# Kernel optimization log

Hardware: AMD Instinct MI355X
Metric: run time of the kernel (lower is better)

The kernel has to match this reference:

```python
import jax, jax.numpy as jnp
import numpy as np
from jax import lax

B, N, IN_DIM = 8, 196, 2048
C = 256          # conv_channels / subspace dim
G = 1            # relation_glimpse


def _dilated_conv(x, w, b, dil):
    # x: [B,N,N,Cin], w: [3,3,Cin,Cout], SAME padding, rhs dilation per source
    y = lax.conv_general_dilated(x, w, window_strides=(1, 1), padding='SAME',
                                 rhs_dilation=dil,
                                 dimension_numbers=('NHWC', 'HWIO', 'NHWC'))
    return y + b


def _rel_map(X):
    # X: [B,N,N,G] -> symmetric add, move glimpse to axis 1, softmax over N*N
    Xs = X + jnp.transpose(X, (0, 2, 1, 3))          # [B,N,N,G]
    m = jnp.transpose(Xs, (0, 3, 2, 1))              # [B,G,N,N]
    bsz, g, n, _ = m.shape
    m = jax.nn.softmax(m.reshape(bsz, g, n * n), axis=2)
    return m.reshape(bsz, g, n, n)


def setup_inputs() -> dict:
    key = jax.random.key(0)
    ks = jax.random.split(key, 8)
    s = lambda *sh: 1.0 / np.sqrt(sh[-2] if len(sh) > 1 else sh[0])
    return {
        'x': jax.random.normal(ks[0], (B, N, IN_DIM), jnp.float32),
        'w_prj': jax.random.normal(ks[1], (IN_DIM, C), jnp.float32) * 0.02,
        'b_prj': jnp.zeros((C,), jnp.float32),
        'w01': jax.random.normal(ks[2], (C, C // 2), jnp.float32) * 0.06,
        'b01': jnp.zeros((C // 2,), jnp.float32),
        'w02': jax.random.normal(ks[3], (C // 2, C // 4), jnp.float32) * 0.09,
        'b02': jnp.zeros((C // 4,), jnp.float32),
        'w03': jax.random.normal(ks[4], (C // 4, G), jnp.float32) * 0.125,
        'b03': jnp.zeros((G,), jnp.float32),
        'w1': jax.random.normal(ks[5], (3, 3, C, C // 2), jnp.float32) * 0.02,
        'b1': jnp.zeros((C // 2,), jnp.float32),
        'w2': jax.random.normal(ks[6], (3, 3, C // 2, C // 4), jnp.float32) * 0.03,
        'b2': jnp.zeros((C // 4,), jnp.float32),
        'w3': jax.random.normal(ks[7], (3, 3, C // 4, G), jnp.float32) * 0.04,
        'b3': jnp.zeros((G,), jnp.float32),
    }


def reference(x, w_prj, b_prj, w01, b01, w02, b02, w03, b03,
              w1, b1, w2, b2, w3, b3):
    # project to subspace: [B,N,C]
    sub = jnp.einsum('bnd,dc->bnc', x, w_prj) + b_prj
    # pairwise outer product: pair[b,i,j,c] = sub[b,i,c]*sub[b,j,c]
    pair = sub[:, :, None, :] * sub[:, None, :, :]          # [B,N,N,C]

    # branch 0: stacked 1x1 convs (pointwise) with relu; dropout = identity (eval)
    X0 = jax.nn.relu(jnp.einsum('bijc,cd->bijd', pair, w01) + b01)
    X0 = jax.nn.relu(jnp.einsum('bijc,cd->bijd', X0, w02) + b02)
    X0 = jax.nn.relu(jnp.einsum('bijc,cd->bijd', X0, w03) + b03)  # [B,N,N,G]
    rel_map0 = _rel_map(X0)                                  # [B,G,N,N]

    # branch 1: stacked 3x3 dilated convs, dilations (1,1),(1,2),(1,4)
    X1 = jax.nn.relu(_dilated_conv(pair, w1, b1, (1, 1)))
    X1 = jax.nn.relu(_dilated_conv(X1, w2, b2, (1, 2)))
    X1 = jax.nn.relu(_dilated_conv(X1, w3, b3, (1, 4)))      # [B,N,N,G]
    rel_map1 = _rel_map(X1)

    # aggregation over glimpses: rel_x = sum_g (map1[g]@x + map0[g]@x) / (2G)
    rel_x = (jnp.einsum('bgij,bjd->bid', rel_map1, x) +
             jnp.einsum('bgij,bjd->bid', rel_map0, x)) / (2.0 * G)
    return rel_x.reshape(x.shape[0], -1)                     # [B, N*in_dim]
```

## Files before the change

### kernel.cpp

```cpp
#include <hip/hip_runtime.h>
#include <cmath>

#define N_TOK 196
#define NPX   38416
#define CDIM  256

typedef _Float16 f16;
typedef __attribute__((ext_vector_type(8))) _Float16 half8;
typedef __attribute__((ext_vector_type(4))) float f32x4;

__global__ __launch_bounds__(256) void proj_mfma(
    const float* __restrict__ A,
    const float* __restrict__ B,
    float* __restrict__ P)
{
    __shared__ f16 As[128 * 40];
    __shared__ f16 Bs[128 * 40];
    int tid = threadIdx.x;
    int n0 = blockIdx.x * 128, m0 = blockIdx.y * 128;
    int kz = blockIdx.z;
    int wave = tid >> 6, lane = tid & 63;
    int quad = lane >> 4, l16 = lane & 15;

    f32x4 zero = {0.f, 0.f, 0.f, 0.f};
    f32x4 acc[2][8];
    #pragma unroll
    for (int mt = 0; mt < 2; ++mt)
        #pragma unroll
        for (int nt = 0; nt < 8; ++nt) acc[mt][nt] = zero;

    for (int k0 = kz * 256; k0 < kz * 256 + 256; k0 += 32) {
        __syncthreads();
        #pragma unroll
        for (int s = 0; s < 4; ++s) {
            int idx = tid + s * 256;
            int m = idx >> 3, kq = idx & 7;
            int gm = m0 + m;
            float4 v = make_float4(0.f, 0.f, 0.f, 0.f);
            if (gm < 1568) v = *(const float4*)(A + (size_t)gm * 2048 + k0 + kq * 4);
            f16* d = As + m * 40 + kq * 4;
            d[0] = (f16)v.x; d[1] = (f16)v.y; d[2] = (f16)v.z; d[3] = (f16)v.w;
        }
        #pragma unroll
        for (int s = 0; s < 4; ++s) {
            int idx = tid + s * 256;
            int nq = idx & 31, kk = idx >> 5;
            float4 v = *(const float4*)(B + (size_t)(k0 + kk) * 256 + n0 + nq * 4);
            Bs[(nq * 4 + 0) * 40 + kk] = (f16)v.x;
            Bs[(nq * 4 + 1) * 40 + kk] = (f16)v.y;
            Bs[(nq * 4 + 2) * 40 + kk] = (f16)v.z;
            Bs[(nq * 4 + 3) * 40 + kk] = (f16)v.w;
        }
        __syncthreads();
        half8 a[2];
        #pragma unroll
        for (int mt = 0; mt < 2; ++mt)
            a[mt] = *(const half8*)(As + (wave * 32 + mt * 16 + l16) * 40 + quad * 8);
        #pragma unroll
        for (int nt = 0; nt < 8; ++nt) {
            half8 bf = *(const half8*)(Bs + (nt * 16 + l16) * 40 + quad * 8);
            acc[0][nt] = __builtin_amdgcn_mfma_f32_16x16x32_f16(a[0], bf, acc[0][nt], 0, 0, 0);
            acc[1][nt] = __builtin_amdgcn_mfma_f32_16x16x32_f16(a[1], bf, acc[1][nt], 0, 0, 0);
        }
    }
    float* Pz = P + (size_t)kz * 401408;
    #pragma unroll
    for (int mt = 0; mt < 2; ++mt) {
        #pragma unroll
        for (int nt = 0; nt < 8; ++nt) {
            int gn = n0 + nt * 16 + l16;
            #pragma unroll
            for (int r = 0; r < 4; ++r) {
                int gm = m0 + wave * 32 + mt * 16 + quad * 4 + r;
                if (gm < 1568) Pz[(size_t)gm * 256 + gn] = acc[mt][nt][r];
            }
        }
    }
}

__global__ void reduce_subh(const float* __restrict__ P,
                            const float* __restrict__ bias,
                            f16* __restrict__ subh)
{
    int e = blockIdx.x * 256 + threadIdx.x;
    if (e >= 401408) return;
    float s = bias[e & 255];
    #pragma unroll
    for (int z = 0; z < 8; ++z) s += P[(size_t)z * 401408 + e];
    subh[e] = (f16)s;
}

__global__ void cvt_wt(const float* __restrict__ w, f16* __restrict__ wt,
                       int Kc, int D, int total)
{
    int e = blockIdx.x * 256 + threadIdx.x;
    if (e >= total) return;
    int td = Kc * D;
    int tap = e / td, r = e - tap * td;
    int c = r / D, d = r - c * D;
    wt[(size_t)(tap * D + d) * Kc + c] = (f16)w[e];
}

__global__ void cvt_wfrag(const float* __restrict__ w, f16* __restrict__ wf,
                          int Kc, int D, int taps)
{
    int tiles = D >> 4, kch = Kc >> 5;
    int total = taps * tiles * kch * 64;
    int e = blockIdx.x * 256 + threadIdx.x;
    if (e >= total) return;
    int lane = e & 63;
    int rest = e >> 6;
    int k = rest % kch; rest /= kch;
    int tile = rest % tiles;
    int tap = rest / tiles;
    int l16 = lane & 15, quad = lane >> 4;
    const float* src = w + ((size_t)tap * Kc + k * 32 + quad * 8) * D + tile * 16 + l16;
    f16* dst = wf + (size_t)e * 8;
    #pragma unroll
    for (int j = 0; j < 8; ++j) dst[j] = (f16)src[(size_t)j * D];
}

__global__ __launch_bounds__(256) void cvt_xT(const float* __restrict__ x,
                                              f16* __restrict__ xht)
{
    __shared__ float t[32][33];
    int b = blockIdx.z;
    int i0 = blockIdx.y * 32, n0 = blockIdx.x * 32;
    const float* xb = x + (size_t)b * 196 * 2048;
    for (int e = threadIdx.x; e < 1024; e += 256) {
        int r = e >> 5, c = e & 31;
        int gi = i0 + r;
        t[r][c] = (gi < 196) ? xb[(size_t)gi * 2048 + n0 + c] : 0.f;
    }
    __syncthreads();
    f16* xb2 = xht + (size_t)b * 2048 * 200;
    for (int e = threadIdx.x; e < 1024; e += 256) {
        int nl = e >> 5, il = e & 31;
        int gi = i0 + il, gn = n0 + nl;
        if (gi < 200) xb2[(size_t)gn * 200 + gi] = (f16)t[il][nl];
    }
}

__global__ __launch_bounds__(256, 2) void conv1_mfma(
    const f16* __restrict__ sub_h,
    const f16* __restrict__ w1f,
    const float* __restrict__ b1,
    f16* __restrict__ Y1h)
{
    __shared__ f16 sh[17408];
    f16* SJ = sh;
    f16* SI = sh + 8976;
    f16* OT = sh;

    int b = blockIdx.z;
    int i0 = blockIdx.y * 8, j0 = blockIdx.x * 32;
    int tid = threadIdx.x;
    const f16* subB = sub_h + (size_t)b * N_TOK * CDIM;

    uint4 zz = make_uint4(0, 0, 0, 0);
    for (int e = tid; e < 1088; e += 256) {
        int r = e >> 5, q = e & 31;
        int gj = j0 - 1 + r;
        uint4 v = zz;
        if (gj >= 0 && gj < N_TOK) v = *(const uint4*)(subB + gj * CDIM + q * 8);
        *(uint4*)(SJ + r * 264 + q * 8) = v;
    }
    for (int e = tid; e < 320; e += 256) {
        int r = e >> 5, q = e & 31;
        int gi = i0 - 1 + r;
        uint4 v = zz;
        if (gi >= 0 && gi < N_TOK) v = *(const uint4*)(subB + gi * CDIM + q * 8);
        *(uint4*)(SI + r * 264 + q * 8) = v;
    }
    __syncthreads();

    int wave = tid >> 6, lane = tid & 63;
    int quad = lane >> 4, l16 = lane & 15;
    int p  = wave >> 1;
    int dh = wave & 1;
    int d0 = dh * 64;

    float bias_r[4];
    #pragma unroll
    for (int n = 0; n < 4; ++n) bias_r[n] = b1[d0 + n * 16 + l16];

    const f16* wbase = w1f + (size_t)lane * 8 + (size_t)dh * 4 * 4096;

    f32x4 zero = {0.f, 0.f, 0.f, 0.f};
    f32x4 acc[8][4];
    #pragma unroll
    for (int m = 0; m < 8; ++m)
        #pragma unroll
        for (int n = 0; n < 4; ++n) acc[m][n] = zero;

    for (int k = 0; k < 8; ++k) {
        int c0 = k * 32;
        half8 si[6];
        #pragma unroll
        for (int r = 0; r < 6; ++r)
            si[r] = *(const half8*)(SI + (p * 4 + r) * 264 + c0 + quad * 8);
        half8 sj[2][3];
        #pragma unroll
        for (int jf = 0; jf < 2; ++jf)
            #pragma unroll
            for (int dd = 0; dd < 3; ++dd)
                sj[jf][dd] = *(const half8*)(SJ + (jf * 16 + l16 + dd) * 264 + c0 + quad * 8);

        #pragma unroll
        for (int dj = 0; dj < 3; ++dj) {
            half8 bf[3][4];
            #pragma unroll
            for (int di = 0; di < 3; ++di)
                #pragma unroll
                for (int n = 0; n < 4; ++n)
                    bf[di][n] = *(const half8*)(wbase + (size_t)(di * 3 + dj) * 32768
                                                + n * 4096 + k * 512);
            #pragma unroll
            for (int r = 0; r < 6; ++r) {
                half8 a0 = si[r] * sj[0][dj];
                half8 a1 = si[r] * sj[1][dj];
                #pragma unroll
                for (int di = 0; di < 3; ++di) {
                    int i = r - di;
                    if (i < 0 || i > 3) continue;
                    #pragma unroll
                    for (int n = 0; n < 4; ++n) {
                        acc[i * 2 + 0][n] = __builtin_amdgcn_mfma_f32_16x16x32_f16(
                            a0, bf[di][n], acc[i * 2 + 0][n], 0, 0, 0);
                        acc[i * 2 + 1][n] = __builtin_amdgcn_mfma_f32_16x16x32_f16(
                            a1, bf[di][n], acc[i * 2 + 1][n], 0, 0, 0);
                    }
                }
            }
        }
    }

    __syncthreads();
    f16* Yb = Y1h + (size_t)b * NPX * 128;
    #pragma unroll
    for (int ph = 0; ph < 2; ++ph) {
        if (p == ph) {
            #pragma unroll
            for (int i = 0; i < 4; ++i)
                #pragma unroll
                for (int jf = 0; jf < 2; ++jf) {
                    int m = i * 2 + jf;
                    #pragma unroll
                    for (int n = 0; n < 4; ++n) {
                        int dl = d0 + n * 16 + l16;
                        #pragma unroll
                        for (int r = 0; r < 4; ++r) {
                            int pxl = i * 32 + jf * 16 + quad * 4 + r;
                            OT[pxl * 136 + dl] = (f16)fmaxf(acc[m][n][r] + bias_r[n], 0.f);
                        }
                    }
                }
        }
        __syncthreads();
        for (int e = tid; e < 2048; e += 256) {
            int pxl = e >> 4, q = e & 15;
            int gi = i0 + ph * 4 + (pxl >> 5), gj = j0 + (pxl & 31);
            if (gi < N_TOK && gj < N_TOK)
                *(uint4*)(Yb + ((size_t)gi * N_TOK + gj) * 128 + q * 8) =
                    *(const uint4*)(OT + pxl * 136 + q * 8);
        }
        __syncthreads();
    }
}

__global__ __launch_bounds__(256, 2) void conv2_mfma(
    const f16* __restrict__ Y1h, const f16* __restrict__ w2f,
    const float* __restrict__ b2, f16* __restrict__ Y2h)
{
    __shared__ f16 sh[19584];
    f16* Ys = sh;
    f16* OT = sh;

    int b = blockIdx.z;
    int i0 = blockIdx.y * 2, j0 = blockIdx.x * 32;
    int tid = threadIdx.x;
    const f16* Yb = Y1h + (size_t)b * NPX * 128;

    uint4 zz = make_uint4(0, 0, 0, 0);
    for (int e = tid; e < 2304; e += 256) {
        int ir = e / 576, rem = e - ir * 576;
        int jq = rem >> 4, q = rem & 15;
        int gi = i0 - 1 + ir, gj = j0 - 2 + jq;
        uint4 v = zz;
        if (gi >= 0 && gi < N_TOK && gj >= 0 && gj < N_TOK)
            v = *(const uint4*)(Yb + ((size_t)gi * N_TOK + gj) * 128 + q * 8);
        *(uint4*)(Ys + (ir * 36 + jq) * 136 + q * 8) = v;
    }
    __syncthreads();

    int wave = tid >> 6, lane = tid & 63;
    int quad = lane >> 4, l16 = lane & 15;
    int ii = wave >> 1, jb = (wave & 1) * 16;

    const f16* wbase = w2f + (size_t)lane * 8;

    f32x4 zero = {0.f, 0.f, 0.f, 0.f};
    f32x4 acc[4] = {zero, zero, zero, zero};

    #pragma unroll
    for (int tap = 0; tap < 9; ++tap) {
        int di = tap / 3 - 1, dj2 = (tap % 3 - 1) * 2;
        #pragma unroll
        for (int k = 0; k < 4; ++k) {
            int c0 = k * 32;
            half8 a = *(const half8*)(Ys + ((ii + di + 1) * 36 + jb + l16 + dj2 + 2) * 136
                                      + c0 + quad * 8);
            #pragma unroll
            for (int n = 0; n < 4; ++n) {
                half8 bf = *(const half8*)(wbase + (size_t)tap * 8192 + n * 2048 + k * 512);
                acc[n] = __builtin_amdgcn_mfma_f32_16x16x32_f16(a, bf, acc[n], 0, 0, 0);
            }
        }
    }
    __syncthreads();
    #pragma unroll
    for (int n = 0; n < 4; ++n) {
        int d = n * 16 + l16;
        float bias = b2[d];
        #pragma unroll
        for (int r = 0; r < 4; ++r) {
            int px = ii * 32 + jb + quad * 4 + r;
            OT[px * 72 + d] = (f16)fmaxf(acc[n][r] + bias, 0.f);
        }
    }
    __syncthreads();
    f16* Zb = Y2h + (size_t)b * NPX * 64;
    for (int e = tid; e < 512; e += 256) {
        int px = e >> 3, q = e & 7;
        int i = i0 + (px >> 5), j = j0 + (px & 31);
        if (j < N_TOK)
            *(uint4*)(Zb + ((size_t)i * N_TOK + j) * 64 + q * 8) =
                *(const uint4*)(OT + px * 72 + q * 8);
    }
}

__global__ __launch_bounds__(256) void conv3_h(
    const f16* __restrict__ Y2h, const float* __restrict__ w3,
    const float* __restrict__ b3, float* __restrict__ X1)
{
    __shared__ float w[576];
    int b = blockIdx.y;
    const f16* Yb = Y2h + (size_t)b * NPX * 64;
    for (int e = threadIdx.x; e < 576; e += 256) w[e] = w3[e];
    __syncthreads();
    int px = blockIdx.x * 256 + threadIdx.x;
    if (px >= NPX) return;
    int i = px / 196, j = px - i * 196;
    float s = b3[0];
    for (int tap = 0; tap < 9; ++tap) {
        int gi = i + tap / 3 - 1, gj = j + (tap % 3 - 1) * 4;
        if (gi < 0 || gi >= N_TOK || gj < 0 || gj >= N_TOK) continue;
        const half8* src = (const half8*)(Yb + ((size_t)gi * N_TOK + gj) * 64);
        const float* wt = w + tap * 64;
        #pragma unroll
        for (int q = 0; q < 8; ++q) {
            half8 h = src[q];
            #pragma unroll
            for (int e = 0; e < 8; ++e) s += (float)h[e] * wt[q * 8 + e];
        }
    }
    X1[(size_t)b * NPX + px] = fmaxf(s, 0.f);
}

__global__ __launch_bounds__(256, 2) void branch0_mfma(
    const f16* __restrict__ sub_h,
    const f16* __restrict__ w01t,
    const float* __restrict__ b01,
    const f16* __restrict__ w02t,
    const float* __restrict__ b02,
    const float* __restrict__ w03, const float* __restrict__ b03,
    float* __restrict__ X0)
{
    __shared__ f16 sh[32000];
    __shared__ float W3s[64];
    f16* SJ = sh;
    f16* SI = sh + 8448;
    f16* BW = sh + 9472;
    f16* H1 = sh + 14592;
    f16* H2 = sh;

    int b = blockIdx.z;
    int i0 = blockIdx.y * 4, j0 = blockIdx.x * 32;
    int tid = threadIdx.x;
    const f16* subB = sub_h + (size_t)b * N_TOK * CDIM;

    uint4 zz = make_uint4(0, 0, 0, 0);
    for (int e = tid; e < 1024; e += 256) {
        int r = e >> 5, q = e & 31;
        int gj = j0 + r;
        uint4 v = zz;
        if (gj < N_TOK) v = *(const uint4*)(subB + gj * CDIM + q * 8);
        *(uint4*)(SJ + r * 264 + q * 8) = v;
    }
    if (tid < 128) {
        int r = tid >> 5, q = tid & 31;
        int gi = i0 + r;
        uint4 v = zz;
        if (gi < N_TOK) v = *(const uint4*)(subB + gi * CDIM + q * 8);
        *(uint4*)(SI + r * 256 + q * 8) = v;
    }
    if (tid < 64) W3s[tid] = w03[tid];

    int wave = tid >> 6, lane = tid & 63;
    int quad = lane >> 4, l16 = lane & 15;
    int ii = wave;

    f32x4 zero = {0.f, 0.f, 0.f, 0.f};
    f32x4 acc[2][8];
    #pragma unroll
    for (int t = 0; t < 2; ++t)
        #pragma unroll
        for (int n = 0; n < 8; ++n) acc[t][n] = zero;

    for (int c0 = 0; c0 < 256; c0 += 32) {
        __syncthreads();
        for (int e = tid; e < 512; e += 256) {
            int d = e >> 2, q = e & 3;
            *(uint4*)(BW + d * 40 + q * 8) =
                *(const uint4*)(w01t + (size_t)d * 256 + c0 + q * 8);
        }
        __syncthreads();
        half8 sib = *(const half8*)(SI + ii * 256 + c0 + quad * 8);
        half8 a0 = sib * *(const half8*)(SJ + l16 * 264 + c0 + quad * 8);
        half8 a1 = sib * *(const half8*)(SJ + (l16 + 16) * 264 + c0 + quad * 8);
        #pragma unroll
        for (int n = 0; n < 8; ++n) {
            half8 bf = *(const half8*)(BW + (n * 16 + l16) * 40 + quad * 8);
            acc[0][n] = __builtin_amdgcn_mfma_f32_16x16x32_f16(a0, bf, acc[0][n], 0, 0, 0);
            acc[1][n] = __builtin_amdgcn_mfma_f32_16x16x32_f16(a1, bf, acc[1][n], 0, 0, 0);
        }
    }
    #pragma unroll
    for (int t = 0; t < 2; ++t)
        #pragma unroll
        for (int n = 0; n < 8; ++n) {
            int d = n * 16 + l16;
            float bias = b01[d];
            #pragma unroll
            for (int r = 0; r < 4; ++r) {
                int px = ii * 32 + t * 16 + quad * 4 + r;
                H1[px * 136 + d] = (f16)fmaxf(acc[t][n][r] + bias, 0.f);
            }
        }

    f32x4 acc2[2][4];
    #pragma unroll
    for (int t = 0; t < 2; ++t)
        #pragma unroll
        for (int n = 0; n < 4; ++n) acc2[t][n] = zero;

    for (int c0 = 0; c0 < 128; c0 += 32) {
        __syncthreads();
        {
            int d = tid >> 2, q = tid & 3;
            if (d < 64)
                *(uint4*)(BW + d * 40 + q * 8) =
                    *(const uint4*)(w02t + (size_t)d * 128 + c0 + q * 8);
        }
        __syncthreads();
        half8 a0 = *(const half8*)(H1 + (ii * 32 + l16) * 136 + c0 + quad * 8);
        half8 a1 = *(const half8*)(H1 + (ii * 32 + 16 + l16) * 136 + c0 + quad * 8);
        #pragma unroll
        for (int n = 0; n < 4; ++n) {
            half8 bf = *(const half8*)(BW + (n * 16 + l16) * 40 + quad * 8);
            acc2[0][n] = __builtin_amdgcn_mfma_f32_16x16x32_f16(a0, bf, acc2[0][n], 0, 0, 0);
            acc2[1][n] = __builtin_amdgcn_mfma_f32_16x16x32_f16(a1, bf, acc2[1][n], 0, 0, 0);
        }
    }
    #pragma unroll
    for (int t = 0; t < 2; ++t)
        #pragma unroll
        for (int n = 0; n < 4; ++n) {
            int e = n * 16 + l16;
            float bias = b02[e];
            #pragma unroll
            for (int r = 0; r < 4; ++r) {
                int px = ii * 32 + t * 16 + quad * 4 + r;
                H2[px * 72 + e] = (f16)fmaxf(acc2[t][n][r] + bias, 0.f);
            }
        }
    __syncthreads();
    if (tid < 128) {
        int px = tid;
        float s = b03[0];
        const f16* h = H2 + px * 72;
        #pragma unroll 8
        for (int c = 0; c < 64; ++c) s += (float)h[c] * W3s[c];
        int i = i0 + (px >> 5), j = j0 + (px & 31);
        if (j < N_TOK)
            X0[(size_t)b * NPX + i * N_TOK + j] = fmaxf(s, 0.f);
    }
}

__global__ __launch_bounds__(1024) void symsoftmax(float* __restrict__ X0,
                                                   float* __restrict__ X1)
{
    __shared__ float red[32];
    __shared__ float red2[32];
    float* X = (blockIdx.y ? X1 : X0) + (long long)blockIdx.x * NPX;
    int tid = threadIdx.x;
    float v[38];
    float mx = -3.0e38f;
    #pragma unroll
    for (int p = 0; p < 38; ++p) {
        int e = tid + p * 1024;
        if (e < NPX) {
            int i = e / 196, j = e - i * 196;
            float t = X[e] + X[j * 196 + i];
            v[p] = t;
            mx = fmaxf(mx, t);
        } else v[p] = -3.0e38f;
    }
    #pragma unroll
    for (int off = 32; off > 0; off >>= 1) mx = fmaxf(mx, __shfl_xor(mx, off));
    if ((tid & 63) == 0) red[tid >> 6] = mx;
    __syncthreads();
    if (tid < 64) {
        float m = (tid < 16) ? red[tid] : -3.0e38f;
        #pragma unroll
        for (int off = 8; off > 0; off >>= 1) m = fmaxf(m, __shfl_xor(m, off));
        if (tid == 0) red[0] = m;
    }
    __syncthreads();
    mx = red[0];
    float s = 0.f;
    #pragma unroll
    for (int p = 0; p < 38; ++p) {
        int e = tid + p * 1024;
        float ex = (e < NPX) ? expf(v[p] - mx) : 0.f;
        v[p] = ex;
        s += ex;
    }
    #pragma unroll
    for (int off = 32; off > 0; off >>= 1) s += __shfl_xor(s, off);
    if ((tid & 63) == 0) red2[tid >> 6] = s;
    __syncthreads();
    if (tid < 64) {
        float m = (tid < 16) ? red2[tid] : 0.f;
        #pragma unroll
        for (int off = 8; off > 0; off >>= 1) m += __shfl_xor(m, off);
        if (tid == 0) red2[0] = m;
    }
    __syncthreads();
    float scale = 0.5f / red2[0];
    #pragma unroll
    for (int p = 0; p < 38; ++p) {
        int e = tid + p * 1024;
        if (e < NPX) X[e] = v[p] * scale;
    }
}

__global__ void combine_ph(const float* __restrict__ X0,
                           const float* __restrict__ X1,
                           f16* __restrict__ Ph)
{
    int e = blockIdx.x * 256 + threadIdx.x;
    if (e >= 8 * 196 * 200) return;
    int j = e % 200;
    int row = e / 200;
    f16 v = (f16)0.f;
    if (j < 196) {
        int src = row * 196 + j;
        v = (f16)((X0[src] + X1[src]) * 512.0f);
    }
    Ph[e] = v;
}

__global__ __launch_bounds__(256, 2) void gemm_out(
    const f16* __restrict__ Ph, const f16* __restrict__ xht,
    float* __restrict__ out)
{
    __shared__ f16 As[64 * 72];
    __shared__ f16 Bs[128 * 72];
    int b = blockIdx.z;
    int n0 = blockIdx.x * 128, m0 = blockIdx.y * 64;
    int tid = threadIdx.x;
    const f16* Pb = Ph + (size_t)b * 196 * 200;
    const f16* xb = xht + (size_t)b * 2048 * 200;

    int wave = tid >> 6, lane = tid & 63;
    int quad = lane >> 4, l16 = lane & 15;

    f32x4 zero = {0.f, 0.f, 0.f, 0.f};
    f32x4 acc[8];
    #pragma unroll
    for (int n = 0; n < 8; ++n) acc[n] = zero;

    uint4 zz = make_uint4(0, 0, 0, 0);
    for (int k0 = 0; k0 < 256; k0 += 64) {
        __syncthreads();
        for (int e = tid; e < 512; e += 256) {
            int r = e >> 3, q = e & 7;
            int gm = m0 + r, k = k0 + q * 8;
            uint4 v = zz;
            if (gm < 196 && k < 200) v = *(const uint4*)(Pb + (size_t)gm * 200 + k);
            *(uint4*)(As + r * 72 + q * 8) = v;
        }
        for (int e = tid; e < 1024; e += 256) {
            int r = e >> 3, q = e & 7;
            int k = k0 + q * 8;
            uint4 v = zz;
            if (k < 200) v = *(const uint4*)(xb + (size_t)(n0 + r) * 200 + k);
            *(uint4*)(Bs + r * 72 + q * 8) = v;
        }
        __syncthreads();
        #pragma unroll
        for (int ks = 0; ks < 2; ++ks) {
            half8 a = *(const half8*)(As + (wave * 16 + l16) * 72 + ks * 32 + quad * 8);
            #pragma unroll
            for (int n = 0; n < 8; ++n) {
                half8 bf = *(const half8*)(Bs + (n * 16 + l16) * 72 + ks * 32 + quad * 8);
                acc[n] = __builtin_amdgcn_mfma_f32_16x16x32_f16(a, bf, acc[n], 0, 0, 0);
            }
        }
    }
    int m_base = m0 + wave * 16 + quad * 4;
    float* ob = out + (size_t)b * 196 * 2048;
    #pragma unroll
    for (int n = 0; n < 8; ++n) {
        int gn = n0 + n * 16 + l16;
        #pragma unroll
        for (int r = 0; r < 4; ++r) {
            int gm = m_base + r;
            if (gm < 196) ob[(size_t)gm * 2048 + gn] = acc[n][r] * (1.0f / 512.0f);
        }
    }
}

extern "C" void kernel_launch(void* const* d_in, const int* in_sizes, int n_in,
                              void* d_out, int out_size, void* d_ws, size_t ws_size,
                              hipStream_t stream)
{
    (void)in_sizes; (void)n_in; (void)out_size; (void)ws_size;
    const float* x     = (const float*)d_in[0];
    const float* w_prj = (const float*)d_in[1];
    const float* b_prj = (const float*)d_in[2];
    const float* w01   = (const float*)d_in[3];
    const float* b01   = (const float*)d_in[4];
    const float* w02   = (const float*)d_in[5];
    const float* b02   = (const float*)d_in[6];
    const float* w03   = (const float*)d_in[7];
    const float* b03   = (const float*)d_in[8];
    const float* w1    = (const float*)d_in[9];
    const float* b1    = (const float*)d_in[10];
    const float* w2    = (const float*)d_in[11];
    const float* b2    = (const float*)d_in[12];
    const float* w3    = (const float*)d_in[13];
    const float* b3    = (const float*)d_in[14];

    char* W = (char*)d_ws;
    float* part = (float*)(W + 0);
    float* X0   = (float*)(W + 12845056);
    float* X1   = (float*)(W + 14074368);
    f16*   subh = (f16*)(W + 15303680);
    f16*   w1f  = (f16*)(W + 16106496);
    f16*   w2f  = (f16*)(W + 16696320);
    f16*   w01t = (f16*)(W + 16843776);
    f16*   w02t = (f16*)(W + 16909312);
    f16*   Ph   = (f16*)(W + 16925696);
    f16*   xht  = (f16*)(W + 17552896);
    f16*   Y1h  = (f16*)(W + 24106496);
    f16*   Y2h  = (f16*)(W + 102782464);

    proj_mfma<<<dim3(2, 13, 8), 256, 0, stream>>>(x, w_prj, part);
    reduce_subh<<<dim3(1568), 256, 0, stream>>>(part, b_prj, subh);

    cvt_wfrag<<<dim3(144), 256, 0, stream>>>(w1, w1f, 256, 128, 9);
    cvt_wfrag<<<dim3(36),  256, 0, stream>>>(w2, w2f, 128, 64, 9);
    cvt_wt<<<dim3(128),  256, 0, stream>>>(w01, w01t, 256, 128, 32768);
    cvt_wt<<<dim3(32),   256, 0, stream>>>(w02, w02t, 128, 64, 8192);
    cvt_xT<<<dim3(64, 7, 8), 256, 0, stream>>>(x, xht);

    branch0_mfma<<<dim3(7, 49, 8), 256, 0, stream>>>(
        subh, w01t, b01, w02t, b02, w03, b03, X0);

    conv1_mfma<<<dim3(7, 25, 8), 256, 0, stream>>>(subh, w1f, b1, Y1h);
    conv2_mfma<<<dim3(7, 98, 8), 256, 0, stream>>>(Y1h, w2f, b2, Y2h);
    conv3_h<<<dim3(151, 8), 256, 0, stream>>>(Y2h, w3, b3, X1);

    symsoftmax<<<dim3(8, 2), 1024, 0, stream>>>(X0, X1);

    combine_ph<<<dim3(1225), 256, 0, stream>>>(X0, X1, Ph);

    gemm_out<<<dim3(16, 4, 8), 256, 0, stream>>>(Ph, xht, (float*)d_out);
}
```

Baseline: 541.4 us.

## Tile conv3 through shared memory and feed branch0 weights as pre-swizzled fragments

conv3 previously gave each thread one pixel and had it read all 9 taps straight from global memory. It now stages a haloed 10x40 tile of Y2 in LDS, splits the 64 channels across 8 lanes, and combines their partial sums with shuffles. Branch0 no longer copies weight slices into LDS with two barriers per k-step. It loads MFMA-fragment-ordered weights, produced by cvt_wfrag, directly from global memory, which also shrinks its LDS footprint. The cost is more global or cache traffic for the B operand in branch0, and a larger LDS allocation in conv3.

```diff
diff --git a/kernel.cpp b/kernel.cpp
--- a/kernel.cpp
+++ b/kernel.cpp
@@ -88,17 +88,6 @@
     #pragma unroll
     for (int z = 0; z < 8; ++z) s += P[(size_t)z * 401408 + e];
     subh[e] = (f16)s;
-}
-
-__global__ void cvt_wt(const float* __restrict__ w, f16* __restrict__ wt,
-                       int Kc, int D, int total)
-{
-    int e = blockIdx.x * 256 + threadIdx.x;
-    if (e >= total) return;
-    int td = Kc * D;
-    int tap = e / td, r = e - tap * td;
-    int c = r / D, d = r - c * D;
-    wt[(size_t)(tap * D + d) * Kc + c] = (f16)w[e];
 }
 
 __global__ void cvt_wfrag(const float* __restrict__ w, f16* __restrict__ wf,
@@ -339,49 +328,66 @@
     }
 }
 
-__global__ __launch_bounds__(256) void conv3_h(
+__global__ __launch_bounds__(256) void conv3_s(
     const f16* __restrict__ Y2h, const float* __restrict__ w3,
     const float* __restrict__ b3, float* __restrict__ X1)
 {
-    __shared__ float w[576];
-    int b = blockIdx.y;
+    __shared__ f16 Ys[10 * 40 * 68];
+    __shared__ float ws[576];
+    int b = blockIdx.z;
+    int i0 = blockIdx.y * 8, j0 = blockIdx.x * 32;
+    int tid = threadIdx.x;
     const f16* Yb = Y2h + (size_t)b * NPX * 64;
-    for (int e = threadIdx.x; e < 576; e += 256) w[e] = w3[e];
-    __syncthreads();
-    int px = blockIdx.x * 256 + threadIdx.x;
-    if (px >= NPX) return;
-    int i = px / 196, j = px - i * 196;
-    float s = b3[0];
-    for (int tap = 0; tap < 9; ++tap) {
-        int gi = i + tap / 3 - 1, gj = j + (tap % 3 - 1) * 4;
-        if (gi < 0 || gi >= N_TOK || gj < 0 || gj >= N_TOK) continue;
-        const half8* src = (const half8*)(Yb + ((size_t)gi * N_TOK + gj) * 64);
-        const float* wt = w + tap * 64;
-        #pragma unroll
-        for (int q = 0; q < 8; ++q) {
-            half8 h = src[q];
-            #pragma unroll
-            for (int e = 0; e < 8; ++e) s += (float)h[e] * wt[q * 8 + e];
-        }
-    }
-    X1[(size_t)b * NPX + px] = fmaxf(s, 0.f);
+    for (int e = tid; e < 576; e += 256) ws[e] = w3[e];
+    uint4 zz = make_uint4(0, 0, 0, 0);
+    for (int e = tid; e < 3200; e += 256) {
+        int r = e / 320, rem = e - r * 320;
+        int jq = rem >> 3, q = rem & 7;
+        int gi = i0 - 1 + r, gj = j0 - 4 + jq;
+        uint4 v = zz;
+        if (gi >= 0 && gi < N_TOK && gj >= 0 && gj < N_TOK)
+            v = *(const uint4*)(Yb + ((size_t)gi * N_TOK + gj) * 64 + q * 8);
+        *(uint4*)(Ys + (r * 40 + jq) * 68 + q * 8) = v;
+    }
+    __syncthreads();
+    int q = tid & 7, jl = (tid >> 3) & 31;
+    float* Xb = X1 + (size_t)b * NPX;
+    float bb = b3[0];
+    #pragma unroll
+    for (int il = 0; il < 8; ++il) {
+        float s = 0.f;
+        #pragma unroll
+        for (int tap = 0; tap < 9; ++tap) {
+            int di = tap / 3 - 1, dj4 = (tap % 3 - 1) * 4;
+            half8 h = *(const half8*)(Ys + ((il + 1 + di) * 40 + jl + 4 + dj4) * 68 + q * 8);
+            #pragma unroll
+            for (int e = 0; e < 8; ++e) s += (float)h[e] * ws[tap * 64 + q * 8 + e];
+        }
+        s += __shfl_xor(s, 1);
+        s += __shfl_xor(s, 2);
+        s += __shfl_xor(s, 4);
+        if (q == 0) {
+            int gi = i0 + il, gj = j0 + jl;
+            if (gi < N_TOK && gj < N_TOK)
+                Xb[gi * N_TOK + gj] = fmaxf(s + bb, 0.f);
+        }
+    }
 }
 
 __global__ __launch_bounds__(256, 2) void branch0_mfma(
     const f16* __restrict__ sub_h,
-    const f16* __restrict__ w01t,
+    const f16* __restrict__ w01f,
     const float* __restrict__ b01,
-    const f16* __restrict__ w02t,
+    const f16* __restrict__ w02f,
     const float* __restrict__ b02,
     const float* __restrict__ w03, const float* __restrict__ b03,
     float* __restrict__ X0)
 {
-    __shared__ f16 sh[32000];
+    __shared__ f16 sh[26880];
     __shared__ float W3s[64];
     f16* SJ = sh;
     f16* SI = sh + 8448;
-    f16* BW = sh + 9472;
-    f16* H1 = sh + 14592;
+    f16* H1 = sh + 9472;
     f16* H2 = sh;
 
     int b = blockIdx.z;
@@ -405,6 +411,7 @@
         *(uint4*)(SI + r * 256 + q * 8) = v;
     }
     if (tid < 64) W3s[tid] = w03[tid];
+    __syncthreads();
 
     int wave = tid >> 6, lane = tid & 63;
     int quad = lane >> 4, l16 = lane & 15;
@@ -417,20 +424,15 @@
         #pragma unroll
         for (int n = 0; n < 8; ++n) acc[t][n] = zero;
 
-    for (int c0 = 0; c0 < 256; c0 += 32) {
-        __syncthreads();
-        for (int e = tid; e < 512; e += 256) {
-            int d = e >> 2, q = e & 3;
-            *(uint4*)(BW + d * 40 + q * 8) =
-                *(const uint4*)(w01t + (size_t)d * 256 + c0 + q * 8);
-        }
-        __syncthreads();
+    const f16* w1base = w01f + (size_t)lane * 8;
+    for (int k = 0; k < 8; ++k) {
+        int c0 = k * 32;
         half8 sib = *(const half8*)(SI + ii * 256 + c0 + quad * 8);
         half8 a0 = sib * *(const half8*)(SJ + l16 * 264 + c0 + quad * 8);
         half8 a1 = sib * *(const half8*)(SJ + (l16 + 16) * 264 + c0 + quad * 8);
         #pragma unroll
         for (int n = 0; n < 8; ++n) {
-            half8 bf = *(const half8*)(BW + (n * 16 + l16) * 40 + quad * 8);
+            half8 bf = *(const half8*)(w1base + n * 4096 + k * 512);
             acc[0][n] = __builtin_amdgcn_mfma_f32_16x16x32_f16(a0, bf, acc[0][n], 0, 0, 0);
             acc[1][n] = __builtin_amdgcn_mfma_f32_16x16x32_f16(a1, bf, acc[1][n], 0, 0, 0);
         }
@@ -447,6 +449,7 @@
                 H1[px * 136 + d] = (f16)fmaxf(acc[t][n][r] + bias, 0.f);
             }
         }
+    __syncthreads();
 
     f32x4 acc2[2][4];
     #pragma unroll
@@ -454,20 +457,14 @@
         #pragma unroll
         for (int n = 0; n < 4; ++n) acc2[t][n] = zero;
 
-    for (int c0 = 0; c0 < 128; c0 += 32) {
-        __syncthreads();
-        {
-            int d = tid >> 2, q = tid & 3;
-            if (d < 64)
-                *(uint4*)(BW + d * 40 + q * 8) =
-                    *(const uint4*)(w02t + (size_t)d * 128 + c0 + q * 8);
-        }
-        __syncthreads();
+    const f16* w2base = w02f + (size_t)lane * 8;
+    for (int k = 0; k < 4; ++k) {
+        int c0 = k * 32;
         half8 a0 = *(const half8*)(H1 + (ii * 32 + l16) * 136 + c0 + quad * 8);
         half8 a1 = *(const half8*)(H1 + (ii * 32 + 16 + l16) * 136 + c0 + quad * 8);
         #pragma unroll
         for (int n = 0; n < 4; ++n) {
-            half8 bf = *(const half8*)(BW + (n * 16 + l16) * 40 + quad * 8);
+            half8 bf = *(const half8*)(w2base + n * 2048 + k * 512);
             acc2[0][n] = __builtin_amdgcn_mfma_f32_16x16x32_f16(a0, bf, acc2[0][n], 0, 0, 0);
             acc2[1][n] = __builtin_amdgcn_mfma_f32_16x16x32_f16(a1, bf, acc2[1][n], 0, 0, 0);
         }
@@ -660,8 +657,8 @@
     f16*   subh = (f16*)(W + 15303680);
     f16*   w1f  = (f16*)(W + 16106496);
     f16*   w2f  = (f16*)(W + 16696320);
-    f16*   w01t = (f16*)(W + 16843776);
-    f16*   w02t = (f16*)(W + 16909312);
+    f16*   w01f = (f16*)(W + 16843776);
+    f16*   w02f = (f16*)(W + 16909312);
     f16*   Ph   = (f16*)(W + 16925696);
     f16*   xht  = (f16*)(W + 17552896);
     f16*   Y1h  = (f16*)(W + 24106496);
@@ -672,16 +669,16 @@
 
     cvt_wfrag<<<dim3(144), 256, 0, stream>>>(w1, w1f, 256, 128, 9);
     cvt_wfrag<<<dim3(36),  256, 0, stream>>>(w2, w2f, 128, 64, 9);
-    cvt_wt<<<dim3(128),  256, 0, stream>>>(w01, w01t, 256, 128, 32768);
-    cvt_wt<<<dim3(32),   256, 0, stream>>>(w02, w02t, 128, 64, 8192);
+    cvt_wfrag<<<dim3(16),  256, 0, stream>>>(w01, w01f, 256, 128, 1);
+    cvt_wfrag<<<dim3(4),   256, 0, stream>>>(w02, w02f, 128, 64, 1);
     cvt_xT<<<dim3(64, 7, 8), 256, 0, stream>>>(x, xht);
 
     branch0_mfma<<<dim3(7, 49, 8), 256, 0, stream>>>(
-        subh, w01t, b01, w02t, b02, w03, b03, X0);
+        subh, w01f, b01, w02f, b02, w03, b03, X0);
 
     conv1_mfma<<<dim3(7, 25, 8), 256, 0, stream>>>(subh, w1f, b1, Y1h);
     conv2_mfma<<<dim3(7, 98, 8), 256, 0, stream>>>(Y1h, w2f, b2, Y2h);
-    conv3_h<<<dim3(151, 8), 256, 0, stream>>>(Y2h, w3, b3, X1);
+    conv3_s<<<dim3(7, 25, 8), 256, 0, stream>>>(Y2h, w3, b3, X1);
 
     symsoftmax<<<dim3(8, 2), 1024, 0, stream>>>(X0, X1);
 
```

Result: slower. 563.1 us (+4.0%).
